# Kernel optimization log

Hardware: AMD Instinct MI355X
Metric: run time of the kernel (lower is better)

## Reference

```python
import jax, jax.numpy as jnp
import numpy as np

N_NODES = 100000
N_EDGES = 1600000
IN_FEATS = 256
OUT_DIM = 128


def setup_inputs() -> dict:
    key = jax.random.key(0)
    k_x, k_e, k_w = jax.random.split(key, 3)
    x = jax.random.normal(k_x, (N_NODES, IN_FEATS), dtype=jnp.float32)
    edge_index = jax.random.randint(k_e, (2, N_EDGES), 0, N_NODES, dtype=jnp.int64)
    # Glorot-ish init for the GCN weight
    W = jax.random.normal(k_w, (IN_FEATS, OUT_DIM), dtype=jnp.float32) * (1.0 / np.sqrt(IN_FEATS))
    b = jnp.zeros((OUT_DIM,), dtype=jnp.float32)
    return {"x": x, "edge_index": edge_index, "W": W, "b": b}


def reference(x, edge_index, W, b):
    N = x.shape[0]
    # GCN with self-loops and symmetric normalization (PyG gcn_norm)
    self_loops = jnp.arange(N, dtype=edge_index.dtype)
    row = jnp.concatenate([edge_index[0], self_loops])  # source nodes
    col = jnp.concatenate([edge_index[1], self_loops])  # target nodes
    deg = jnp.zeros((N,), dtype=x.dtype).at[col].add(1.0)
    deg_inv_sqrt = jnp.where(deg > 0, jax.lax.rsqrt(jnp.maximum(deg, 1.0)), 0.0)
    norm = deg_inv_sqrt[row] * deg_inv_sqrt[col]  # [E+N]
    # Linear transform first (small GEMM), then sparse aggregation
    h = x @ W + b                                  # [N, out_dim]
    msg = h[row] * norm[:, None]                   # gather + scale, [E+N, out_dim]
    out = jax.ops.segment_sum(msg, col, num_segments=N)  # scatter-add
    # relu; dropout is identity in eval mode
    return jax.nn.relu(out)
```

## Files before the change

### kernel.cpp

```cpp
#include <hip/hip_runtime.h>

typedef __attribute__((ext_vector_type(8))) short short8;
typedef __attribute__((ext_vector_type(4))) float f32x4;

#define IN_F 256
#define OUT_F 128
#define NPB 256
#define MAXCAP 5120

__device__ __forceinline__ float bf2f(unsigned int u16) {
    union { unsigned int i; float f; } v; v.i = u16 << 16; return v.f;
}
__device__ __forceinline__ unsigned short f2bf(float f) {
    union { float f; unsigned int i; } v; v.f = f;
    unsigned int u = v.i;
    return (unsigned short)((u + 0x7fffu + ((u >> 16) & 1u)) >> 16);
}

__global__ __launch_bounds__(256) void k_bin(const int* __restrict__ row, const int* __restrict__ col,
                                             int* __restrict__ bcur, int* __restrict__ ebuf,
                                             int E, int NBr, int chunk) {
    __shared__ int hist[512];
    __shared__ int cbase[512];
    int t = threadIdx.x;
    int e0 = blockIdx.x * chunk;
    int e1 = e0 + chunk; if (e1 > E) e1 = E;

    for (int i = t; i < NBr; i += 256) hist[i] = 0;
    __syncthreads();
    for (int i = e0 + t; i < e1; i += 256)
        atomicAdd(&hist[col[i] >> 8], 1);
    __syncthreads();
    for (int i = t; i < NBr; i += 256) {
        int h = hist[i];
        cbase[i] = h ? atomicAdd(&bcur[i], h) : 0;
    }
    __syncthreads();
    for (int i = t; i < NBr; i += 256) hist[i] = 0;
    __syncthreads();
    for (int i = e0 + t; i < e1; i += 256) {
        int c = col[i];
        int r = row[i];
        int b = c >> 8;
        int p = atomicAdd(&hist[b], 1) + cbase[b];
        ebuf[(size_t)b * MAXCAP + p] = (r << 8) | (c & 255);
    }
}

__global__ __launch_bounds__(256) void k_fine(const int* __restrict__ bcur, const int* __restrict__ ebuf,
                                              int* __restrict__ offs, int* __restrict__ deg,
                                              float* __restrict__ dis, int* __restrict__ srci, int N) {
    __shared__ int dl[256];
    __shared__ int sc[256];
    int b = blockIdx.x;
    int t = threadIdx.x;
    int count = bcur[b];
    const int* eb = ebuf + (size_t)b * MAXCAP;

    dl[t] = 0;
    __syncthreads();
    for (int i = t; i < count; i += 256)
        atomicAdd(&dl[eb[i] & 255], 1);
    __syncthreads();
    int myDeg = dl[t];
    sc[t] = myDeg; __syncthreads();
    for (int off = 1; off < 256; off <<= 1) {
        int a = (t >= off) ? sc[t - off] : 0;
        __syncthreads();
        sc[t] += a;
        __syncthreads();
    }
    int excl = sc[t] - myDeg;
    int node = (b << 8) + t;
    int bbase = b * MAXCAP;
    if (node < N) {
        offs[node] = bbase + excl;
        deg[node] = myDeg;
        dis[node] = rsqrtf((float)myDeg + 1.0f);
    }
    dl[t] = excl;
    __syncthreads();
    for (int i = t; i < count; i += 256) {
        int p = eb[i];
        int pos = atomicAdd(&dl[p & 255], 1);
        srci[bbase + pos] = p >> 8;
    }
}

__global__ __launch_bounds__(256) void k_transposeW(const float* __restrict__ W,
                                                    unsigned short* __restrict__ Wt,
                                                    unsigned short* __restrict__ hb, int N) {
    int idx = blockIdx.x * 256 + threadIdx.x;
    if (idx < IN_F * OUT_F) {
        int k = idx >> 7;
        int n = idx & 127;
        Wt[n * IN_F + k] = f2bf(W[idx]);
    }
    if (idx < OUT_F) hb[(size_t)N * OUT_F + idx] = 0;
}

__global__ __launch_bounds__(256) void k_gemm(const float* __restrict__ x,
                                              const unsigned short* __restrict__ Wt,
                                              const float* __restrict__ bias,
                                              const float* __restrict__ dis,
                                              unsigned short* __restrict__ hb, int nrows) {
    int wave = threadIdx.x >> 6;
    int lane = threadIdx.x & 63;
    int m = lane & 15;
    int quad = lane >> 4;

    int row0 = blockIdx.x * 128 + wave * 32;
    int nm1 = nrows - 1;
    int rA = row0 + m;      if (rA > nm1) rA = nm1;
    int rB = row0 + 16 + m; if (rB > nm1) rB = nm1;

    const float4* pa = (const float4*)(x + (size_t)rA * IN_F) + 2 * quad;
    const float4* pb = (const float4*)(x + (size_t)rB * IN_F) + 2 * quad;
    const short8* wf = (const short8*)Wt + (size_t)m * 32 + quad;

    f32x4 acc[2][8];
#pragma unroll
    for (int t = 0; t < 2; t++)
#pragma unroll
        for (int ct = 0; ct < 8; ct++) acc[t][ct] = (f32x4){0.f, 0.f, 0.f, 0.f};

    float4 a0 = pa[0], a1 = pa[1];
    float4 b0 = pb[0], b1 = pb[1];
    short8 w[8];
#pragma unroll
    for (int ct = 0; ct < 8; ct++) w[ct] = wf[ct * 512];

#pragma unroll
    for (int i = 0; i < 8; i++) {
        float4 na0 = {}, na1 = {}, nb0 = {}, nb1 = {};
        short8 nw[8] = {};
        if (i < 7) {
            na0 = pa[8 * (i + 1)];     na1 = pa[8 * (i + 1) + 1];
            nb0 = pb[8 * (i + 1)];     nb1 = pb[8 * (i + 1) + 1];
#pragma unroll
            for (int ct = 0; ct < 8; ct++) nw[ct] = wf[ct * 512 + 4 * (i + 1)];
        }
        short8 af, bf;
        af[0] = (short)f2bf(a0.x); af[1] = (short)f2bf(a0.y);
        af[2] = (short)f2bf(a0.z); af[3] = (short)f2bf(a0.w);
        af[4] = (short)f2bf(a1.x); af[5] = (short)f2bf(a1.y);
        af[6] = (short)f2bf(a1.z); af[7] = (short)f2bf(a1.w);
        bf[0] = (short)f2bf(b0.x); bf[1] = (short)f2bf(b0.y);
        bf[2] = (short)f2bf(b0.z); bf[3] = (short)f2bf(b0.w);
        bf[4] = (short)f2bf(b1.x); bf[5] = (short)f2bf(b1.y);
        bf[6] = (short)f2bf(b1.z); bf[7] = (short)f2bf(b1.w);
#pragma unroll
        for (int ct = 0; ct < 8; ct++)
            acc[0][ct] = __builtin_amdgcn_mfma_f32_16x16x32_bf16(af, w[ct], acc[0][ct], 0, 0, 0);
#pragma unroll
        for (int ct = 0; ct < 8; ct++)
            acc[1][ct] = __builtin_amdgcn_mfma_f32_16x16x32_bf16(bf, w[ct], acc[1][ct], 0, 0, 0);
        a0 = na0; a1 = na1; b0 = nb0; b1 = nb1;
#pragma unroll
        for (int ct = 0; ct < 8; ct++) w[ct] = nw[ct];
    }

    float bv[8];
#pragma unroll
    for (int ct = 0; ct < 8; ct++) bv[ct] = bias[ct * 16 + m];

    int orow0 = blockIdx.x * 128 + wave * 32 + quad * 4;
#pragma unroll
    for (int t = 0; t < 2; t++) {
#pragma unroll
        for (int r = 0; r < 4; r++) {
            int orow = orow0 + t * 16 + r;
            if (orow < nrows) {
                float dr = dis[orow];
#pragma unroll
                for (int ct = 0; ct < 8; ct++)
                    hb[(size_t)orow * OUT_F + ct * 16 + m] = f2bf((acc[t][ct][r] + bv[ct]) * dr);
            }
        }
    }
}

__global__ __launch_bounds__(256) void k_agg(const unsigned short* __restrict__ hb,
                                             const float* __restrict__ dis,
                                             const int* __restrict__ offs, const int* __restrict__ deg,
                                             const int* __restrict__ srci,
                                             float* __restrict__ out, int n) {
    int node = blockIdx.x * 4 + (threadIdx.x >> 6);
    if (node >= n) return;
    int lane = threadIdx.x & 63;

    unsigned int v = *(const unsigned int*)(hb + (size_t)node * OUT_F + lane * 2);
    float ax = bf2f(v & 0xffffu);
    float ay = bf2f(v >> 16);

    int start = offs[node];
    int cnt = deg[node];

    for (int base = 0; base < cnt; base += 64) {
        int mm = cnt - base; if (mm > 64) mm = 64;
        int e = (lane < mm) ? srci[start + base + lane] : n;
        int mround = (mm + 7) & ~7;
        for (int j = 0; j < mround; j += 8) {
            int rr[8];
#pragma unroll
            for (int k = 0; k < 8; k++) rr[k] = __shfl(e, j + k);
            unsigned int w[8];
#pragma unroll
            for (int k = 0; k < 8; k++)
                w[k] = *(const unsigned int*)(hb + (size_t)rr[k] * OUT_F + lane * 2);
#pragma unroll
            for (int k = 0; k < 8; k++) {
                ax += bf2f(w[k] & 0xffffu);
                ay += bf2f(w[k] >> 16);
            }
        }
    }

    float di = dis[node];
    float2 o;
    o.x = fmaxf(ax * di, 0.f);
    o.y = fmaxf(ay * di, 0.f);
    *(float2*)(out + (size_t)node * OUT_F + lane * 2) = o;
}

static inline size_t alignup(size_t v, size_t a) { return (v + a - 1) & ~(a - 1); }

extern "C" void kernel_launch(void* const* d_in, const int* in_sizes, int n_in,
                              void* d_out, int out_size, void* d_ws, size_t ws_size,
                              hipStream_t stream) {
    const float* x  = (const float*)d_in[0];
    const int* ei   = (const int*)d_in[1];
    const float* W  = (const float*)d_in[2];
    const float* b  = (const float*)d_in[3];
    float* out      = (float*)d_out;

    const int N = in_sizes[0] / IN_F;
    const int E = in_sizes[1] / 2;
    const int* rowp = ei;
    const int* colp = ei + E;

    const int NBr = (N + NPB - 1) / NPB;

    char* ws = (char*)d_ws;
    size_t off = 0;
    int*   bcur   = (int*)(ws + off);   off = alignup(off + (size_t)NBr * 4, 256);
    int*   deg    = (int*)(ws + off);   off = alignup(off + (size_t)N * 4, 256);
    float* dis    = (float*)(ws + off); off = alignup(off + (size_t)N * 4, 256);
    int*   offs   = (int*)(ws + off);   off = alignup(off + (size_t)N * 4, 256);
    unsigned short* Wt = (unsigned short*)(ws + off); off = alignup(off + (size_t)IN_F * OUT_F * 2, 256);
    int*   ebuf   = (int*)(ws + off);   off = alignup(off + (size_t)NBr * MAXCAP * 4, 256);
    int*   srci   = (int*)(ws + off);   off = alignup(off + (size_t)NBr * MAXCAP * 4, 256);
    unsigned short* hb = (unsigned short*)(ws + off); off = alignup(off + (size_t)(N + 1) * OUT_F * 2, 256);

    (void)hipMemsetAsync(bcur, 0, (size_t)NBr * 4, stream);

    int chunk = (E + 511) / 512;
    k_bin<<<512, 256, 0, stream>>>(rowp, colp, bcur, ebuf, E, NBr, chunk);
    k_fine<<<NBr, 256, 0, stream>>>(bcur, ebuf, offs, deg, dis, srci, N);

    k_transposeW<<<(IN_F * OUT_F + 255) / 256, 256, 0, stream>>>(W, Wt, hb, N);
    k_gemm<<<(N + 127) / 128, 256, 0, stream>>>(x, Wt, b, dis, hb, N);

    k_agg<<<(N + 3) / 4, 256, 0, stream>>>(hb, dis, offs, deg, srci, out, N);
}
```

Measured before the change: 313.3 us.

## Stage GEMM x tiles into LDS via async global_load_lds double buffering

Measured after the change: 314.1 us. About the same (+0.3%).

```diff
diff --git a/kernel.cpp b/kernel.cpp
--- a/kernel.cpp
+++ b/kernel.cpp
@@ -104,61 +104,84 @@
                                               const float* __restrict__ bias,
                                               const float* __restrict__ dis,
                                               unsigned short* __restrict__ hb, int nrows) {
-    int wave = threadIdx.x >> 6;
-    int lane = threadIdx.x & 63;
+    __shared__ float4 xs[2][1024];
+
+    int t = threadIdx.x;
+    int wave = t >> 6;
+    int lane = t & 63;
     int m = lane & 15;
     int quad = lane >> 4;
-
-    int row0 = blockIdx.x * 128 + wave * 32;
+    int row0 = blockIdx.x * 128;
     int nm1 = nrows - 1;
-    int rA = row0 + m;      if (rA > nm1) rA = nm1;
-    int rB = row0 + 16 + m; if (rB > nm1) rB = nm1;
-
-    const float4* pa = (const float4*)(x + (size_t)rA * IN_F) + 2 * quad;
-    const float4* pb = (const float4*)(x + (size_t)rB * IN_F) + 2 * quad;
+
     const short8* wf = (const short8*)Wt + (size_t)m * 32 + quad;
 
+#define STAGE(ks, buf)                                                                     \
+    do {                                                                                   \
+        _Pragma("unroll")                                                                  \
+        for (int j = 0; j < 4; j++) {                                                      \
+            int s = wave * 256 + j * 64 + lane;                                            \
+            int r = s >> 3;                                                                \
+            int cg = (s & 7) ^ (r & 7);                                                    \
+            int gr = row0 + r; if (gr > nm1) gr = nm1;                                     \
+            const float* ga = x + (size_t)gr * IN_F + (ks) * 32 + cg * 4;                  \
+            __builtin_amdgcn_global_load_lds(                                              \
+                (const __attribute__((address_space(1))) unsigned int*)(const void*)ga,    \
+                (__attribute__((address_space(3))) unsigned int*)(void*)&xs[buf][wave * 256 + j * 64], \
+                16, 0, 0);                                                                 \
+        }                                                                                  \
+    } while (0)
+
     f32x4 acc[2][8];
 #pragma unroll
-    for (int t = 0; t < 2; t++)
-#pragma unroll
-        for (int ct = 0; ct < 8; ct++) acc[t][ct] = (f32x4){0.f, 0.f, 0.f, 0.f};
-
-    float4 a0 = pa[0], a1 = pa[1];
-    float4 b0 = pb[0], b1 = pb[1];
-    short8 w[8];
-#pragma unroll
-    for (int ct = 0; ct < 8; ct++) w[ct] = wf[ct * 512];
+    for (int tt = 0; tt < 2; tt++)
+#pragma unroll
+        for (int ct = 0; ct < 8; ct++) acc[tt][ct] = (f32x4){0.f, 0.f, 0.f, 0.f};
+
+    int rA = wave * 32 + m;
+    int eA = rA & 7;
+    int uA = rA * 8;
+    int uB = (rA + 16) * 8;
+    int c0 = (2 * quad) ^ eA;
+    int c1 = (2 * quad + 1) ^ eA;
+
+    STAGE(0, 0);
 
 #pragma unroll
     for (int i = 0; i < 8; i++) {
-        float4 na0 = {}, na1 = {}, nb0 = {}, nb1 = {};
-        short8 nw[8] = {};
-        if (i < 7) {
-            na0 = pa[8 * (i + 1)];     na1 = pa[8 * (i + 1) + 1];
-            nb0 = pb[8 * (i + 1)];     nb1 = pb[8 * (i + 1) + 1];
-#pragma unroll
-            for (int ct = 0; ct < 8; ct++) nw[ct] = wf[ct * 512 + 4 * (i + 1)];
-        }
+        short8 w[8];
+#pragma unroll
+        for (int ct = 0; ct < 8; ct++) w[ct] = wf[ct * 512 + i * 4];
+
+        if (i < 7) STAGE(i + 1, (i + 1) & 1);
+
+        if (i < 7) __builtin_amdgcn_s_waitcnt(0x0F7C);
+        else       __builtin_amdgcn_s_waitcnt(0x0F78);
+
+        int buf = i & 1;
+        float4 xa0 = xs[buf][uA + c0];
+        float4 xa1 = xs[buf][uA + c1];
+        float4 xb0 = xs[buf][uB + c0];
+        float4 xb1 = xs[buf][uB + c1];
+
         short8 af, bf;
-        af[0] = (short)f2bf(a0.x); af[1] = (short)f2bf(a0.y);
-        af[2] = (short)f2bf(a0.z); af[3] = (short)f2bf(a0.w);
-        af[4] = (short)f2bf(a1.x); af[5] = (short)f2bf(a1.y);
-        af[6] = (short)f2bf(a1.z); af[7] = (short)f2bf(a1.w);
-        bf[0] = (short)f2bf(b0.x); bf[1] = (short)f2bf(b0.y);
-        bf[2] = (short)f2bf(b0.z); bf[3] = (short)f2bf(b0.w);
-        bf[4] = (short)f2bf(b1.x); bf[5] = (short)f2bf(b1.y);
-        bf[6] = (short)f2bf(b1.z); bf[7] = (short)f2bf(b1.w);
+        af[0] = (short)f2bf(xa0.x); af[1] = (short)f2bf(xa0.y);
+        af[2] = (short)f2bf(xa0.z); af[3] = (short)f2bf(xa0.w);
+        af[4] = (short)f2bf(xa1.x); af[5] = (short)f2bf(xa1.y);
+        af[6] = (short)f2bf(xa1.z); af[7] = (short)f2bf(xa1.w);
+        bf[0] = (short)f2bf(xb0.x); bf[1] = (short)f2bf(xb0.y);
+        bf[2] = (short)f2bf(xb0.z); bf[3] = (short)f2bf(xb0.w);
+        bf[4] = (short)f2bf(xb1.x); bf[5] = (short)f2bf(xb1.y);
+        bf[6] = (short)f2bf(xb1.z); bf[7] = (short)f2bf(xb1.w);
+
 #pragma unroll
         for (int ct = 0; ct < 8; ct++)
             acc[0][ct] = __builtin_amdgcn_mfma_f32_16x16x32_bf16(af, w[ct], acc[0][ct], 0, 0, 0);
 #pragma unroll
         for (int ct = 0; ct < 8; ct++)
             acc[1][ct] = __builtin_amdgcn_mfma_f32_16x16x32_bf16(bf, w[ct], acc[1][ct], 0, 0, 0);
-        a0 = na0; a1 = na1; b0 = nb0; b1 = nb1;
-#pragma unroll
-        for (int ct = 0; ct < 8; ct++) w[ct] = nw[ct];
-    }
+    }
+#undef STAGE
 
     float bv[8];
 #pragma unroll
@@ -166,15 +189,15 @@
 
     int orow0 = blockIdx.x * 128 + wave * 32 + quad * 4;
 #pragma unroll
-    for (int t = 0; t < 2; t++) {
+    for (int tt = 0; tt < 2; tt++) {
 #pragma unroll
         for (int r = 0; r < 4; r++) {
-            int orow = orow0 + t * 16 + r;
+            int orow = orow0 + tt * 16 + r;
             if (orow < nrows) {
                 float dr = dis[orow];
 #pragma unroll
                 for (int ct = 0; ct < 8; ct++)
-                    hb[(size_t)orow * OUT_F + ct * 16 + m] = f2bf((acc[t][ct][r] + bv[ct]) * dr);
+                    hb[(size_t)orow * OUT_F + ct * 16 + m] = f2bf((acc[tt][ct][r] + bv[ct]) * dr);
             }
         }
     }
```
